# Performance work log

Hardware: AMD Instinct MI355X
Metric: run time of the kernel (lower is better)

The kernel has to match this reference:

```python
import jax, jax.numpy as jnp
import numpy as np

CURV = 1.0          # manifold curvature c
HEADS = 4
HEAD_DIM = 32       # (dim-1) // heads = 128 // 4
SCALE = HEAD_DIM ** -0.5
EPS = 1e-7

N_NODES = 50000
N_EDGES = 800000
D = 128             # tangent feature dim (dim - 1)


def log_origin(x, c):
    """Lorentz log map at the origin o=(1/sqrt(c),0,...); returns spatial (d) part of tangent."""
    sc = jnp.sqrt(c)
    x0 = x[..., 0]
    xs = x[..., 1:]
    norm = jnp.sqrt(jnp.sum(xs * xs, axis=-1) + EPS)         # (N,)
    dist = jnp.arccosh(jnp.maximum(sc * x0, 1.0 + EPS)) / sc  # (N,)
    return (dist / norm)[..., None] * xs                      # (N, d)


def exp_origin(vs, c):
    """Lorentz exp map at origin of tangent vector (0, vs); returns point (N, d+1)."""
    sc = jnp.sqrt(c)
    r = jnp.sqrt(jnp.sum(vs * vs, axis=-1) + EPS)  # (N,)
    arg = sc * r
    x0 = jnp.cosh(arg) / sc
    xs = (jnp.sinh(arg) / arg)[..., None] * vs
    return jnp.concatenate([x0[..., None], xs], axis=-1)


def setup_inputs() -> dict:
    key = jax.random.key(0)
    k1, k2, k3, k4, k5, k6, k7 = jax.random.split(key, 7)
    # valid hyperboloid points: x0 = sqrt(1/c + ||xs||^2)
    xs = 0.5 * jax.random.normal(k1, (N_NODES, D), dtype=jnp.float32)
    x0 = jnp.sqrt(1.0 / CURV + jnp.sum(xs * xs, axis=-1, keepdims=True))
    x = jnp.concatenate([x0, xs], axis=-1)  # (N, d+1)
    edge_index = jax.random.randint(k2, (2, N_EDGES), 0, N_NODES, dtype=jnp.int64)
    s = D ** -0.5
    Wq = s * jax.random.normal(k3, (D, D), dtype=jnp.float32)
    Wk = s * jax.random.normal(k4, (D, D), dtype=jnp.float32)
    Wv = s * jax.random.normal(k5, (D, D), dtype=jnp.float32)
    Wo = s * jax.random.normal(k6, (D, D), dtype=jnp.float32)
    bo = jnp.zeros((D,), dtype=jnp.float32)
    return {"x": x, "edge_index": edge_index, "Wq": Wq, "Wk": Wk, "Wv": Wv, "Wo": Wo, "bo": bo}


def reference(x, edge_index, Wq, Wk, Wv, Wo, bo):
    N = x.shape[0]
    row, col = edge_index[0], edge_index[1]
    # map to tangent space at origin, drop the (zero) time component
    x_tan = log_origin(x, CURV)                       # (N, d)
    Q = (x_tan @ Wq.T).reshape(N, HEADS, HEAD_DIM)
    K = (x_tan @ Wk.T).reshape(N, HEADS, HEAD_DIM)
    V = (x_tan @ Wv.T).reshape(N, HEADS, HEAD_DIM)
    # per-edge attention logits, grouped softmax over incoming edges of each target node (col)
    scores = jnp.einsum('ehd,ehd->eh', Q[col], K[row]) * SCALE   # (E, H)
    m = jax.ops.segment_max(scores, col, num_segments=N)         # (N, H)
    e = jnp.exp(scores - m[col])
    denom = jax.ops.segment_sum(e, col, num_segments=N)          # (N, H)
    att = e / denom[col]                                         # (E, H)
    # weighted scatter-sum of values
    agg = jax.ops.segment_sum(att[..., None] * V[row], col, num_segments=N)  # (N, H, hd)
    agg = agg.reshape(N, HEADS * HEAD_DIM)
    out = agg @ Wo.T + bo                                        # (N, d)
    # lift back: prepend zero time component, exp map at origin
    return exp_origin(out, CURV)                                 # (N, d+1)
```

## Files before the change

kernel.cpp:

```cpp
#include <hip/hip_runtime.h>
#include <hip/hip_fp8.h>
#include <math.h>

#define EPS 1e-7f
#define SCALE 0.17677669529663687f
#define MAXDEG 64
#define BIN_EPT 16
#define BIN_EDGES 4096
#define BUCK_CAP 5120
#define NBUCK_MAX 256

typedef _Float16 half2v __attribute__((ext_vector_type(2)));
typedef _Float16 f16x4 __attribute__((ext_vector_type(4)));
typedef _Float16 f16x8 __attribute__((ext_vector_type(8)));
typedef float f32x4 __attribute__((ext_vector_type(4)));
typedef float f32x2 __attribute__((ext_vector_type(2)));

__device__ __forceinline__ void gload16(const void* g, void* l) {
  __builtin_amdgcn_global_load_lds(
      (const __attribute__((address_space(1))) unsigned int*)g,
      (__attribute__((address_space(3))) unsigned int*)l, 16, 0, 0);
}

__global__ __launch_bounds__(256) void zero_cnt(int* __restrict__ bcnt, int n) {
  int i = blockIdx.x * 256 + threadIdx.x;
  if (i < n) bcnt[i] = 0;
}

__global__ __launch_bounds__(256) void prep_kernel(
    const float* __restrict__ x,
    const float* __restrict__ Wq, const float* __restrict__ Wk,
    const float* __restrict__ Wv, const float* __restrict__ Wo,
    _Float16* __restrict__ Wc, _Float16* __restrict__ Wof,
    _Float16* __restrict__ xt,
    const int* __restrict__ col, const int* __restrict__ row,
    unsigned* __restrict__ staging, int* __restrict__ bcnt,
    int bin_nb, int nbuck, int E, int N) {
  __shared__ int hist[NBUCK_MAX];
  __shared__ int rbase[NBUCK_MAX];
  int b = blockIdx.x;
  int tid = threadIdx.x;
  if (b < bin_nb) {
    int e0 = b * BIN_EDGES;
    if (tid < nbuck) hist[tid] = 0;
    __syncthreads();
    int bkt[BIN_EPT], rk[BIN_EPT];
    unsigned pk[BIN_EPT];
#pragma unroll
    for (int j = 0; j < BIN_EPT; j++) {
      int e = e0 + j * 256 + tid;
      if (e < E) {
        int c = col[e];
        int r = row[e];
        int bb = c >> 8;
        bkt[j] = bb;
        pk[j] = ((unsigned)(c & 255) << 16) | (unsigned)r;
        rk[j] = atomicAdd(&hist[bb], 1);
      } else {
        bkt[j] = -1;
        rk[j] = 0;
        pk[j] = 0;
      }
    }
    __syncthreads();
    if (tid < nbuck) rbase[tid] = atomicAdd(&bcnt[tid], hist[tid]);
    __syncthreads();
#pragma unroll
    for (int j = 0; j < BIN_EPT; j++) {
      if (bkt[j] >= 0) {
        int slot = rbase[bkt[j]] + rk[j];
        if (slot < BUCK_CAP)
          staging[(size_t)bkt[j] * BUCK_CAP + slot] = pk[j];
      }
    }
    return;
  }
  b -= bin_nb;
  if (b < 256) {
    int o = b * 256 + tid;
    int j = o >> 7;
    int i = o & 127;
    if (j < 384) {
      const float* W = (j < 128) ? Wq : (j < 256) ? Wk : Wv;
      Wc[o] = (_Float16)W[(j & 127) * 128 + i];
    } else {
      Wof[(j - 384) * 128 + i] = (_Float16)Wo[(j - 384) * 128 + i];
    }
    return;
  }
  int node = (b - 256) * 4 + (tid >> 6);
  if (node >= N) return;
  int lane = tid & 63;
  float2 xs = *reinterpret_cast<const float2*>(&x[(size_t)node * 129 + 1 + lane * 2]);
  float ss = fmaf(xs.x, xs.x, xs.y * xs.y);
#pragma unroll
  for (int o = 32; o >= 1; o >>= 1) ss += __shfl_xor(ss, o, 64);
  float norm = sqrtf(ss + EPS);
  float x0 = x[(size_t)node * 129];
  float xm = fmaxf(x0, 1.0f + EPS);
  float dist = __logf(xm + sqrtf(fmaxf(fmaf(xm, xm, -1.0f), 0.0f)));
  float sc = dist / norm;
  half2v h;
  h.x = (_Float16)(sc * xs.x);
  h.y = (_Float16)(sc * xs.y);
  *reinterpret_cast<half2v*>(&xt[(size_t)node * 128 + lane * 2]) = h;
}

template <int NCHUNKS, int MODE>
__global__ __launch_bounds__(256, 3) void gemm_mfma(
    const _Float16* __restrict__ A,
    const _Float16* __restrict__ B,
    void* __restrict__ C0, void* __restrict__ C1,
    const float* __restrict__ bias, int M,
    const unsigned* __restrict__ staging, const int* __restrict__ bcnt,
    unsigned short* __restrict__ rml, int* __restrict__ cnt, int Mblocks) {
  __shared__ _Float16 Bs[128 * 128];
  __shared__ __align__(16) unsigned char Cs[16384];
  const int bid = blockIdx.x;
  const int tid = threadIdx.x;

  if (MODE == 0 && bid >= Mblocks) {
    int bk = bid - Mblocks;
    unsigned short* slab = (unsigned short*)Bs;
    int* lc = (int*)Cs;
    lc[tid] = 0;
    __syncthreads();
    int ec = bcnt[bk];
    if (ec > BUCK_CAP) ec = BUCK_CAP;
    const unsigned* sg = staging + (size_t)bk * BUCK_CAP;
    for (int i = tid; i < ec; i += 256) {
      unsigned p = sg[i];
      int nl = p >> 16;
      int pos = atomicAdd(&lc[nl], 1);
      if (pos < MAXDEG) slab[nl * MAXDEG + pos] = (unsigned short)(p & 0xFFFF);
    }
    __syncthreads();
    uint4* gs = (uint4*)(rml + (size_t)bk * 256 * MAXDEG);
    const uint4* ls = (const uint4*)slab;
#pragma unroll
    for (int i = 0; i < 8; i++) gs[i * 256 + tid] = ls[i * 256 + tid];
    int c = lc[tid];
    cnt[bk * 256 + tid] = (c > MAXDEG) ? MAXDEG : c;
    return;
  }

  const int wave = tid >> 6;
  const int lane = tid & 63;
  const int wm = wave >> 1, wn = wave & 1;
  const int lrow = lane & 15, q = lane >> 4;
  const int m0 = bid * 64;

#pragma unroll
  for (int j = 0; j < 4; j++) {
    int slot0 = (j * 4 + wave) * 64;
    int p = slot0 + lane;
    int m = p >> 4;
    int kcl = (p & 15) ^ (m & 15);
    int msrc = m0 + m;
    if (msrc > M - 1) msrc = M - 1;
    gload16(A + (size_t)msrc * 128 + kcl * 8, (char*)Bs + (size_t)slot0 * 16);
  }
  __syncthreads();

  f16x8 afr[2][4];
  {
    const f16x8* Av = (const f16x8*)Bs;
#pragma unroll
    for (int mt = 0; mt < 2; mt++) {
      int m = wm * 32 + mt * 16 + lrow;
#pragma unroll
      for (int s = 0; s < 4; s++) {
        int kc = s * 4 + q;
        afr[mt][s] = Av[m * 16 + (kc ^ (m & 15))];
      }
    }
  }
  __syncthreads();

  auto stageB = [&](int c) {
#pragma unroll
    for (int j = 0; j < 8; j++) {
      int slot0 = (j * 4 + wave) * 64;
      int p = slot0 + lane;
      int n = p >> 4;
      int kcl = (p & 15) ^ (n & 15);
      gload16(B + ((size_t)(c * 128 + n)) * 128 + kcl * 8, (char*)Bs + (size_t)slot0 * 16);
    }
  };
  stageB(0);

  f32x4 acc[2][4];
  for (int c = 0; c < NCHUNKS; c++) {
    __syncthreads();

#pragma unroll
    for (int mt = 0; mt < 2; mt++)
#pragma unroll
      for (int nt = 0; nt < 4; nt++) acc[mt][nt] = (f32x4)0.f;

    const f16x8* Bv = (const f16x8*)Bs;
#pragma unroll
    for (int s = 0; s < 4; s++) {
      int kc = s * 4 + q;
      f16x8 bf[4];
#pragma unroll
      for (int nt = 0; nt < 4; nt++) {
        int n = wn * 64 + nt * 16 + lrow;
        bf[nt] = Bv[n * 16 + (kc ^ (n & 15))];
      }
#pragma unroll
      for (int mt = 0; mt < 2; mt++)
#pragma unroll
        for (int nt = 0; nt < 4; nt++)
          acc[mt][nt] = __builtin_amdgcn_mfma_f32_16x16x32_f16(afr[mt][s], bf[nt], acc[mt][nt], 0, 0, 0);
    }

    if (MODE == 0) {
      if (c == 0) {
#pragma unroll
        for (int mt = 0; mt < 2; mt++)
#pragma unroll
          for (int reg = 0; reg < 4; reg++) {
            int r = wm * 32 + mt * 16 + q * 4 + reg;
            int sw = ((r >> 2) & 3) << 5;
#pragma unroll
            for (int nt = 0; nt < 4; nt++) {
              int cl = wn * 64 + nt * 16 + lrow;
              *(_Float16*)(Cs + r * 256 + ((cl * 2) ^ sw)) = (_Float16)acc[mt][nt][reg];
            }
          }
      } else {
        unsigned char* cb = Cs + ((c == 2) ? 8192 : 0);
#pragma unroll
        for (int mt = 0; mt < 2; mt++) {
          int rb = wm * 32 + mt * 16 + q * 4;
          int sw = ((rb >> 2) & 3) << 5;
#pragma unroll
          for (int nt = 0; nt < 4; nt++) {
            int cl = wn * 64 + nt * 16 + lrow;
            int co = cl ^ sw;
            int p01 = __builtin_amdgcn_cvt_pk_fp8_f32(acc[mt][nt][0], acc[mt][nt][1], 0, false);
            int p23 = __builtin_amdgcn_cvt_pk_fp8_f32(acc[mt][nt][2], acc[mt][nt][3], 0, false);
            cb[(rb + 0) * 128 + co] = (unsigned char)(p01);
            cb[(rb + 1) * 128 + co] = (unsigned char)(p01 >> 8);
            cb[(rb + 2) * 128 + co] = (unsigned char)(p23);
            cb[(rb + 3) * 128 + co] = (unsigned char)(p23 >> 8);
          }
        }
      }
    }
    __syncthreads();
    if (c + 1 < NCHUNKS) stageB(c + 1);
    if (MODE == 0) {
      if (c == 0) {
#pragma unroll
        for (int it = 0; it < 4; it++) {
          int off = it * 4096 + tid * 16;
          int r = off >> 8;
          int bo = off & 255;
          int sw = ((r >> 2) & 3) << 5;
          uint4 v = *(const uint4*)(Cs + r * 256 + (bo ^ sw));
          int rg = m0 + r;
          if (rg < M) *(uint4*)((char*)C0 + (size_t)rg * 256 + bo) = v;
        }
      } else if (c == 2) {
#pragma unroll
        for (int it = 0; it < 8; it++) {
          int off = it * 2048 + tid * 8;
          int r = off >> 8;
          int u4 = (off & 255) >> 1;
          int sw = ((r >> 2) & 3) << 5;
          unsigned kw = *(const unsigned*)(Cs + r * 128 + (u4 ^ sw));
          unsigned vw = *(const unsigned*)(Cs + 8192 + r * 128 + (u4 ^ sw));
          int rg = m0 + r;
          if (rg < M) {
            uint2 o;
            o.x = kw;
            o.y = vw;
            *(uint2*)((char*)C1 + (size_t)rg * 256 + (off & 255)) = o;
          }
        }
      }
    }
  }

  if (MODE == 1) {
    float* out = (float*)C0;
    float* rsum = (float*)Cs;
#pragma unroll
    for (int mt = 0; mt < 2; mt++)
#pragma unroll
      for (int nt = 0; nt < 4; nt++) {
        int cl = wn * 64 + nt * 16 + lrow;
        float b = bias[cl];
#pragma unroll
        for (int reg = 0; reg < 4; reg++) acc[mt][nt][reg] += b;
      }
#pragma unroll
    for (int mt = 0; mt < 2; mt++) {
#pragma unroll
      for (int reg = 0; reg < 4; reg++) {
        float s4 = 0.f;
#pragma unroll
        for (int nt = 0; nt < 4; nt++) s4 = fmaf(acc[mt][nt][reg], acc[mt][nt][reg], s4);
#pragma unroll
        for (int o = 8; o >= 1; o >>= 1) s4 += __shfl_xor(s4, o, 16);
        if (lrow == 0) rsum[(wm * 32 + mt * 16 + q * 4 + reg) * 2 + wn] = s4;
      }
    }
    __syncthreads();
#pragma unroll
    for (int mt = 0; mt < 2; mt++) {
#pragma unroll
      for (int reg = 0; reg < 4; reg++) {
        int rl = wm * 32 + mt * 16 + q * 4 + reg;
        int rg = m0 + rl;
        if (rg < M) {
          float tot = rsum[rl * 2] + rsum[rl * 2 + 1];
          float r = sqrtf(tot + EPS);
          float er = __expf(r);
          float em = __expf(-r);
          float s = (er - em) * 0.5f / r;
#pragma unroll
          for (int nt = 0; nt < 4; nt++) {
            int cl = wn * 64 + nt * 16 + lrow;
            out[(size_t)rg * 129 + 1 + cl] = s * acc[mt][nt][reg];
          }
          if (wn == 0 && lrow == 0) out[(size_t)rg * 129] = (er + em) * 0.5f;
        }
      }
    }
  }
}

__global__ __launch_bounds__(256) void attn_kernel(
    const _Float16* __restrict__ Qb,
    const unsigned char* __restrict__ KVI,
    const unsigned short* __restrict__ rml, const int* __restrict__ cnt,
    _Float16* __restrict__ agg, int N) {
  int node = blockIdx.x * 4 + (threadIdx.x >> 6);
  if (node >= N) return;
  int lane = threadIdx.x & 63;
  int par = lane >> 5;
  int hd = lane & 31;
  int qoff = hd * 4;
  f16x4 qh = *reinterpret_cast<const f16x4*>(Qb + (size_t)node * 128 + qoff);
  float q0 = (float)qh[0], q1 = (float)qh[1], q2 = (float)qh[2], q3 = (float)qh[3];
  int deg = cnt[node];
  if (deg > MAXDEG) deg = MAXDEG;
  const unsigned short* el = rml + (size_t)node * MAXDEG;
  float l = 0.f, av0 = 0.f, av1 = 0.f, av2 = 0.f, av3 = 0.f;

  auto dot = [&](uint2 w, float& p, float& v0, float& v1, float& v2, float& v3) {
    f32x2 k01 = __builtin_amdgcn_cvt_pk_f32_fp8((int)w.x, false);
    f32x2 k23 = __builtin_amdgcn_cvt_pk_f32_fp8((int)w.x, true);
    f32x2 va = __builtin_amdgcn_cvt_pk_f32_fp8((int)w.y, false);
    f32x2 vb = __builtin_amdgcn_cvt_pk_f32_fp8((int)w.y, true);
    v0 = va[0]; v1 = va[1]; v2 = vb[0]; v3 = vb[1];
    p = fmaf(q0, k01[0], fmaf(q1, k01[1], fmaf(q2, k23[0], q3 * k23[1])));
  };

  int i = 0;
  for (; i + 8 <= deg; i += 8) {
    int rA = el[i + par], rB = el[i + 2 + par], rC = el[i + 4 + par], rD = el[i + 6 + par];
    uint2 wA = *reinterpret_cast<const uint2*>(KVI + (size_t)rA * 256 + hd * 8);
    uint2 wB = *reinterpret_cast<const uint2*>(KVI + (size_t)rB * 256 + hd * 8);
    uint2 wC = *reinterpret_cast<const uint2*>(KVI + (size_t)rC * 256 + hd * 8);
    uint2 wD = *reinterpret_cast<const uint2*>(KVI + (size_t)rD * 256 + hd * 8);
    float pA, a4, a5, a6, a7;
    float pB, b4, b5, b6, b7;
    float pC, c4, c5, c6, c7;
    float pD, d4, d5, d6, d7;
    dot(wA, pA, a4, a5, a6, a7);
    dot(wB, pB, b4, b5, b6, b7);
    dot(wC, pC, c4, c5, c6, c7);
    dot(wD, pD, d4, d5, d6, d7);
#pragma unroll
    for (int o = 4; o >= 1; o >>= 1) {
      pA += __shfl_xor(pA, o, 8);
      pB += __shfl_xor(pB, o, 8);
      pC += __shfl_xor(pC, o, 8);
      pD += __shfl_xor(pD, o, 8);
    }
    float eA = __expf(pA * SCALE);
    float eB = __expf(pB * SCALE);
    float eC = __expf(pC * SCALE);
    float eD = __expf(pD * SCALE);
    l += (eA + eB) + (eC + eD);
    av0 = fmaf(eA, a4, av0); av0 = fmaf(eB, b4, av0);
    av1 = fmaf(eA, a5, av1); av1 = fmaf(eB, b5, av1);
    av2 = fmaf(eA, a6, av2); av2 = fmaf(eB, b6, av2);
    av3 = fmaf(eA, a7, av3); av3 = fmaf(eB, b7, av3);
    av0 = fmaf(eC, c4, av0); av0 = fmaf(eD, d4, av0);
    av1 = fmaf(eC, c5, av1); av1 = fmaf(eD, d5, av1);
    av2 = fmaf(eC, c6, av2); av2 = fmaf(eD, d6, av2);
    av3 = fmaf(eC, c7, av3); av3 = fmaf(eD, d7, av3);
  }
  for (; i + 2 <= deg; i += 2) {
    int rA = el[i + par];
    uint2 wA = *reinterpret_cast<const uint2*>(KVI + (size_t)rA * 256 + hd * 8);
    float pA, a4, a5, a6, a7;
    dot(wA, pA, a4, a5, a6, a7);
#pragma unroll
    for (int o = 4; o >= 1; o >>= 1) pA += __shfl_xor(pA, o, 8);
    float eA = __expf(pA * SCALE);
    l += eA;
    av0 = fmaf(eA, a4, av0);
    av1 = fmaf(eA, a5, av1);
    av2 = fmaf(eA, a6, av2);
    av3 = fmaf(eA, a7, av3);
  }
  if (i < deg) {
    int r = el[i];
    uint2 wA = *reinterpret_cast<const uint2*>(KVI + (size_t)r * 256 + hd * 8);
    float pA, a4, a5, a6, a7;
    dot(wA, pA, a4, a5, a6, a7);
#pragma unroll
    for (int o = 4; o >= 1; o >>= 1) pA += __shfl_xor(pA, o, 8);
    float e = __expf(pA * SCALE) * (par ? 0.f : 1.f);
    l += e;
    av0 = fmaf(e, a4, av0);
    av1 = fmaf(e, a5, av1);
    av2 = fmaf(e, a6, av2);
    av3 = fmaf(e, a7, av3);
  }
  l += __shfl_xor(l, 32, 64);
  av0 += __shfl_xor(av0, 32, 64);
  av1 += __shfl_xor(av1, 32, 64);
  av2 += __shfl_xor(av2, 32, 64);
  av3 += __shfl_xor(av3, 32, 64);
  if (par == 0) {
    float inv = (l > 0.f) ? 1.0f / l : 0.f;
    f16x4 o4;
    o4[0] = (_Float16)(av0 * inv);
    o4[1] = (_Float16)(av1 * inv);
    o4[2] = (_Float16)(av2 * inv);
    o4[3] = (_Float16)(av3 * inv);
    *reinterpret_cast<f16x4*>(agg + (size_t)node * 128 + qoff) = o4;
  }
}

extern "C" void kernel_launch(void* const* d_in, const int* in_sizes, int n_in,
                              void* d_out, int out_size, void* d_ws, size_t ws_size,
                              hipStream_t stream) {
  const float* x = (const float*)d_in[0];
  const int* ei = (const int*)d_in[1];
  const float* Wq = (const float*)d_in[2];
  const float* Wk = (const float*)d_in[3];
  const float* Wv = (const float*)d_in[4];
  const float* Wo = (const float*)d_in[5];
  const float* bo = (const float*)d_in[6];
  float* out = (float*)d_out;

  const int N = in_sizes[0] / 129;
  const int E = in_sizes[1] / 2;
  const int* row = ei;
  const int* col = ei + E;

  const int nbuck = (N + 255) >> 8;
  const int bin_nb = (E + BIN_EDGES - 1) / BIN_EDGES;

  char* ws = (char*)d_ws;
  size_t off = 0;
  auto alloc = [&](size_t bytes) -> void* {
    off = (off + 255) & ~(size_t)255;
    void* p = ws + off;
    off += bytes;
    return p;
  };
  _Float16* xtan = (_Float16*)alloc((size_t)N * 128 * 2);
  _Float16* qbuf = (_Float16*)alloc((size_t)N * 128 * 2);
  unsigned char* kvi = (unsigned char*)alloc((size_t)N * 256);
  unsigned short* rml = (unsigned short*)alloc((size_t)nbuck * 256 * MAXDEG * 2);
  int* cnt        = (int*)alloc((size_t)nbuck * 256 * 4);
  unsigned* staging = (unsigned*)alloc((size_t)nbuck * BUCK_CAP * 4);
  int* bcnt       = (int*)alloc((size_t)nbuck * 4);
  _Float16* Wc    = (_Float16*)alloc(384 * 128 * 2);
  _Float16* Wof   = (_Float16*)alloc(128 * 128 * 2);

  const int gemm_nb = (N + 63) / 64;

  zero_cnt<<<(nbuck + 255) / 256, 256, 0, stream>>>(bcnt, nbuck);
  prep_kernel<<<bin_nb + 256 + (N + 3) / 4, 256, 0, stream>>>(
      x, Wq, Wk, Wv, Wo, Wc, Wof, xtan, col, row, staging, bcnt, bin_nb, nbuck,
      E, N);
  gemm_mfma<3, 0><<<gemm_nb + nbuck, 256, 0, stream>>>(
      xtan, Wc, qbuf, kvi, nullptr, N, staging, bcnt, rml, cnt, gemm_nb);
  attn_kernel<<<(N + 3) / 4, 256, 0, stream>>>(qbuf, kvi, rml, cnt, xtan, N);
  gemm_mfma<1, 1><<<gemm_nb, 256, 0, stream>>>(
      xtan, Wof, out, nullptr, bo, N, nullptr, nullptr, nullptr, nullptr, 0);
}
```

Measured before the change: 168.5 us.

## Fuse log map into QKV GEMM and output projection into attention kernel

The Lorentz log map now runs inside the QKV GEMM, written straight into the swizzled LDS A tile, so the separate xtan buffer and its global round trip go away. The attention aggregation is fused with the output projection and exp map: each block handles 64 nodes, stages the aggregated values in LDS, then runs the MFMA against Wo read directly from global memory. This removes one kernel launch and the global write and read of the intermediate agg buffer. In exchange the attention phase now uses 64-node blocks with serial per-wave node loops, so fewer blocks are resident, and the B fragments come from global memory rather than LDS.

```diff
diff --git a/kernel.cpp b/kernel.cpp
--- a/kernel.cpp
+++ b/kernel.cpp
@@ -28,14 +28,12 @@
 }
 
 __global__ __launch_bounds__(256) void prep_kernel(
-    const float* __restrict__ x,
     const float* __restrict__ Wq, const float* __restrict__ Wk,
     const float* __restrict__ Wv, const float* __restrict__ Wo,
     _Float16* __restrict__ Wc, _Float16* __restrict__ Wof,
-    _Float16* __restrict__ xt,
     const int* __restrict__ col, const int* __restrict__ row,
     unsigned* __restrict__ staging, int* __restrict__ bcnt,
-    int bin_nb, int nbuck, int E, int N) {
+    int bin_nb, int nbuck, int E) {
   __shared__ int hist[NBUCK_MAX];
   __shared__ int rbase[NBUCK_MAX];
   int b = blockIdx.x;
@@ -76,42 +74,21 @@
     return;
   }
   b -= bin_nb;
-  if (b < 256) {
-    int o = b * 256 + tid;
-    int j = o >> 7;
-    int i = o & 127;
-    if (j < 384) {
-      const float* W = (j < 128) ? Wq : (j < 256) ? Wk : Wv;
-      Wc[o] = (_Float16)W[(j & 127) * 128 + i];
-    } else {
-      Wof[(j - 384) * 128 + i] = (_Float16)Wo[(j - 384) * 128 + i];
-    }
-    return;
-  }
-  int node = (b - 256) * 4 + (tid >> 6);
-  if (node >= N) return;
-  int lane = tid & 63;
-  float2 xs = *reinterpret_cast<const float2*>(&x[(size_t)node * 129 + 1 + lane * 2]);
-  float ss = fmaf(xs.x, xs.x, xs.y * xs.y);
-#pragma unroll
-  for (int o = 32; o >= 1; o >>= 1) ss += __shfl_xor(ss, o, 64);
-  float norm = sqrtf(ss + EPS);
-  float x0 = x[(size_t)node * 129];
-  float xm = fmaxf(x0, 1.0f + EPS);
-  float dist = __logf(xm + sqrtf(fmaxf(fmaf(xm, xm, -1.0f), 0.0f)));
-  float sc = dist / norm;
-  half2v h;
-  h.x = (_Float16)(sc * xs.x);
-  h.y = (_Float16)(sc * xs.y);
-  *reinterpret_cast<half2v*>(&xt[(size_t)node * 128 + lane * 2]) = h;
+  int o = b * 256 + tid;
+  int j = o >> 7;
+  int i = o & 127;
+  if (j < 384) {
+    const float* W = (j < 128) ? Wq : (j < 256) ? Wk : Wv;
+    Wc[o] = (_Float16)W[(j & 127) * 128 + i];
+  } else {
+    Wof[(j - 384) * 128 + i] = (_Float16)Wo[(j - 384) * 128 + i];
+  }
 }
 
-template <int NCHUNKS, int MODE>
-__global__ __launch_bounds__(256, 3) void gemm_mfma(
-    const _Float16* __restrict__ A,
+__global__ __launch_bounds__(256, 3) void qkv_kernel(
+    const float* __restrict__ x,
     const _Float16* __restrict__ B,
-    void* __restrict__ C0, void* __restrict__ C1,
-    const float* __restrict__ bias, int M,
+    void* __restrict__ C0, void* __restrict__ C1, int M,
     const unsigned* __restrict__ staging, const int* __restrict__ bcnt,
     unsigned short* __restrict__ rml, int* __restrict__ cnt, int Mblocks) {
   __shared__ _Float16 Bs[128 * 128];
@@ -119,7 +96,7 @@
   const int bid = blockIdx.x;
   const int tid = threadIdx.x;
 
-  if (MODE == 0 && bid >= Mblocks) {
+  if (bid >= Mblocks) {
     int bk = bid - Mblocks;
     unsigned short* slab = (unsigned short*)Bs;
     int* lc = (int*)Cs;
@@ -150,15 +127,24 @@
   const int lrow = lane & 15, q = lane >> 4;
   const int m0 = bid * 64;
 
-#pragma unroll
-  for (int j = 0; j < 4; j++) {
-    int slot0 = (j * 4 + wave) * 64;
-    int p = slot0 + lane;
-    int m = p >> 4;
-    int kcl = (p & 15) ^ (m & 15);
+  for (int t = 0; t < 16; t++) {
+    int m = (wave << 4) + t;
     int msrc = m0 + m;
     if (msrc > M - 1) msrc = M - 1;
-    gload16(A + (size_t)msrc * 128 + kcl * 8, (char*)Bs + (size_t)slot0 * 16);
+    const float* xr = x + (size_t)msrc * 129;
+    float2 xs = *reinterpret_cast<const float2*>(xr + 1 + lane * 2);
+    float ss = fmaf(xs.x, xs.x, xs.y * xs.y);
+#pragma unroll
+    for (int o = 32; o >= 1; o >>= 1) ss += __shfl_xor(ss, o, 64);
+    float norm = sqrtf(ss + EPS);
+    float xm = fmaxf(xr[0], 1.0f + EPS);
+    float dist = __logf(xm + sqrtf(fmaxf(fmaf(xm, xm, -1.0f), 0.0f)));
+    float sc = dist / norm;
+    half2v h;
+    h.x = (_Float16)(sc * xs.x);
+    h.y = (_Float16)(sc * xs.y);
+    *reinterpret_cast<half2v*>((char*)Bs + m * 256 +
+                               ((((lane >> 2) ^ (m & 15)) << 4) | ((lane & 3) << 2))) = h;
   }
   __syncthreads();
 
@@ -190,7 +176,7 @@
   stageB(0);
 
   f32x4 acc[2][4];
-  for (int c = 0; c < NCHUNKS; c++) {
+  for (int c = 0; c < 3; c++) {
     __syncthreads();
 
 #pragma unroll
@@ -215,143 +201,91 @@
           acc[mt][nt] = __builtin_amdgcn_mfma_f32_16x16x32_f16(afr[mt][s], bf[nt], acc[mt][nt], 0, 0, 0);
     }
 
-    if (MODE == 0) {
-      if (c == 0) {
-#pragma unroll
-        for (int mt = 0; mt < 2; mt++)
-#pragma unroll
-          for (int reg = 0; reg < 4; reg++) {
-            int r = wm * 32 + mt * 16 + q * 4 + reg;
-            int sw = ((r >> 2) & 3) << 5;
-#pragma unroll
-            for (int nt = 0; nt < 4; nt++) {
-              int cl = wn * 64 + nt * 16 + lrow;
-              *(_Float16*)(Cs + r * 256 + ((cl * 2) ^ sw)) = (_Float16)acc[mt][nt][reg];
-            }
-          }
-      } else {
-        unsigned char* cb = Cs + ((c == 2) ? 8192 : 0);
-#pragma unroll
-        for (int mt = 0; mt < 2; mt++) {
-          int rb = wm * 32 + mt * 16 + q * 4;
-          int sw = ((rb >> 2) & 3) << 5;
+    if (c == 0) {
+#pragma unroll
+      for (int mt = 0; mt < 2; mt++)
+#pragma unroll
+        for (int reg = 0; reg < 4; reg++) {
+          int r = wm * 32 + mt * 16 + q * 4 + reg;
+          int sw = ((r >> 2) & 3) << 5;
 #pragma unroll
           for (int nt = 0; nt < 4; nt++) {
             int cl = wn * 64 + nt * 16 + lrow;
-            int co = cl ^ sw;
-            int p01 = __builtin_amdgcn_cvt_pk_fp8_f32(acc[mt][nt][0], acc[mt][nt][1], 0, false);
-            int p23 = __builtin_amdgcn_cvt_pk_fp8_f32(acc[mt][nt][2], acc[mt][nt][3], 0, false);
-            cb[(rb + 0) * 128 + co] = (unsigned char)(p01);
-            cb[(rb + 1) * 128 + co] = (unsigned char)(p01 >> 8);
-            cb[(rb + 2) * 128 + co] = (unsigned char)(p23);
-            cb[(rb + 3) * 128 + co] = (unsigned char)(p23 >> 8);
+            *(_Float16*)(Cs + r * 256 + ((cl * 2) ^ sw)) = (_Float16)acc[mt][nt][reg];
           }
         }
-      }
-    }
-    __syncthreads();
-    if (c + 1 < NCHUNKS) stageB(c + 1);
-    if (MODE == 0) {
-      if (c == 0) {
-#pragma unroll
-        for (int it = 0; it < 4; it++) {
-          int off = it * 4096 + tid * 16;
-          int r = off >> 8;
-          int bo = off & 255;
-          int sw = ((r >> 2) & 3) << 5;
-          uint4 v = *(const uint4*)(Cs + r * 256 + (bo ^ sw));
-          int rg = m0 + r;
-          if (rg < M) *(uint4*)((char*)C0 + (size_t)rg * 256 + bo) = v;
+    } else {
+      unsigned char* cb = Cs + ((c == 2) ? 8192 : 0);
+#pragma unroll
+      for (int mt = 0; mt < 2; mt++) {
+        int rb = wm * 32 + mt * 16 + q * 4;
+        int sw = ((rb >> 2) & 3) << 5;
+#pragma unroll
+        for (int nt = 0; nt < 4; nt++) {
+          int cl = wn * 64 + nt * 16 + lrow;
+          int co = cl ^ sw;
+          int p01 = __builtin_amdgcn_cvt_pk_fp8_f32(acc[mt][nt][0], acc[mt][nt][1], 0, false);
+          int p23 = __builtin_amdgcn_cvt_pk_fp8_f32(acc[mt][nt][2], acc[mt][nt][3], 0, false);
+          cb[(rb + 0) * 128 + co] = (unsigned char)(p01);
+          cb[(rb + 1) * 128 + co] = (unsigned char)(p01 >> 8);
+          cb[(rb + 2) * 128 + co] = (unsigned char)(p23);
+          cb[(rb + 3) * 128 + co] = (unsigned char)(p23 >> 8);
         }
-      } else if (c == 2) {
-#pragma unroll
-        for (int it = 0; it < 8; it++) {
-          int off = it * 2048 + tid * 8;
-          int r = off >> 8;
-          int u4 = (off & 255) >> 1;
-          int sw = ((r >> 2) & 3) << 5;
-          unsigned kw = *(const unsigned*)(Cs + r * 128 + (u4 ^ sw));
-          unsigned vw = *(const unsigned*)(Cs + 8192 + r * 128 + (u4 ^ sw));
-          int rg = m0 + r;
-          if (rg < M) {
-            uint2 o;
-            o.x = kw;
-            o.y = vw;
-            *(uint2*)((char*)C1 + (size_t)rg * 256 + (off & 255)) = o;
-          }
+      }
+    }
+    __syncthreads();
+    if (c + 1 < 3) stageB(c + 1);
+    if (c == 0) {
+#pragma unroll
+      for (int it = 0; it < 4; it++) {
+        int off = it * 4096 + tid * 16;
+        int r = off >> 8;
+        int bo = off & 255;
+        int sw = ((r >> 2) & 3) << 5;
+        uint4 v = *(const uint4*)(Cs + r * 256 + (bo ^ sw));
+        int rg = m0 + r;
+        if (rg < M) *(uint4*)((char*)C0 + (size_t)rg * 256 + bo) = v;
+      }
+    } else if (c == 2) {
+#pragma unroll
+      for (int it = 0; it < 8; it++) {
+        int off = it * 2048 + tid * 8;
+        int r = off >> 8;
+        int u4 = (off & 255) >> 1;
+        int sw = ((r >> 2) & 3) << 5;
+        unsigned kw = *(const unsigned*)(Cs + r * 128 + (u4 ^ sw));
+        unsigned vw = *(const unsigned*)(Cs + 8192 + r * 128 + (u4 ^ sw));
+        int rg = m0 + r;
+        if (rg < M) {
+          uint2 o;
+          o.x = kw;
+          o.y = vw;
+          *(uint2*)((char*)C1 + (size_t)rg * 256 + (off & 255)) = o;
         }
       }
     }
   }
-
-  if (MODE == 1) {
-    float* out = (float*)C0;
-    float* rsum = (float*)Cs;
-#pragma unroll
-    for (int mt = 0; mt < 2; mt++)
-#pragma unroll
-      for (int nt = 0; nt < 4; nt++) {
-        int cl = wn * 64 + nt * 16 + lrow;
-        float b = bias[cl];
-#pragma unroll
-        for (int reg = 0; reg < 4; reg++) acc[mt][nt][reg] += b;
-      }
-#pragma unroll
-    for (int mt = 0; mt < 2; mt++) {
-#pragma unroll
-      for (int reg = 0; reg < 4; reg++) {
-        float s4 = 0.f;
-#pragma unroll
-        for (int nt = 0; nt < 4; nt++) s4 = fmaf(acc[mt][nt][reg], acc[mt][nt][reg], s4);
-#pragma unroll
-        for (int o = 8; o >= 1; o >>= 1) s4 += __shfl_xor(s4, o, 16);
-        if (lrow == 0) rsum[(wm * 32 + mt * 16 + q * 4 + reg) * 2 + wn] = s4;
-      }
-    }
-    __syncthreads();
-#pragma unroll
-    for (int mt = 0; mt < 2; mt++) {
-#pragma unroll
-      for (int reg = 0; reg < 4; reg++) {
-        int rl = wm * 32 + mt * 16 + q * 4 + reg;
-        int rg = m0 + rl;
-        if (rg < M) {
-          float tot = rsum[rl * 2] + rsum[rl * 2 + 1];
-          float r = sqrtf(tot + EPS);
-          float er = __expf(r);
-          float em = __expf(-r);
-          float s = (er - em) * 0.5f / r;
-#pragma unroll
-          for (int nt = 0; nt < 4; nt++) {
-            int cl = wn * 64 + nt * 16 + lrow;
-            out[(size_t)rg * 129 + 1 + cl] = s * acc[mt][nt][reg];
-          }
-          if (wn == 0 && lrow == 0) out[(size_t)rg * 129] = (er + em) * 0.5f;
-        }
-      }
-    }
-  }
 }
 
-__global__ __launch_bounds__(256) void attn_kernel(
+__global__ __launch_bounds__(256) void attn_out_kernel(
     const _Float16* __restrict__ Qb,
     const unsigned char* __restrict__ KVI,
     const unsigned short* __restrict__ rml, const int* __restrict__ cnt,
-    _Float16* __restrict__ agg, int N) {
-  int node = blockIdx.x * 4 + (threadIdx.x >> 6);
-  if (node >= N) return;
-  int lane = threadIdx.x & 63;
-  int par = lane >> 5;
-  int hd = lane & 31;
-  int qoff = hd * 4;
-  f16x4 qh = *reinterpret_cast<const f16x4*>(Qb + (size_t)node * 128 + qoff);
-  float q0 = (float)qh[0], q1 = (float)qh[1], q2 = (float)qh[2], q3 = (float)qh[3];
-  int deg = cnt[node];
-  if (deg > MAXDEG) deg = MAXDEG;
-  const unsigned short* el = rml + (size_t)node * MAXDEG;
-  float l = 0.f, av0 = 0.f, av1 = 0.f, av2 = 0.f, av3 = 0.f;
-
-  auto dot = [&](uint2 w, float& p, float& v0, float& v1, float& v2, float& v3) {
+    const _Float16* __restrict__ Wof,
+    const float* __restrict__ bias,
+    float* __restrict__ out, int N) {
+  __shared__ __align__(16) _Float16 Ags[64 * 128];
+  __shared__ float rsum[64 * 2];
+  const int tid = threadIdx.x;
+  const int wave = tid >> 6;
+  const int lane = tid & 63;
+  const int blk = blockIdx.x;
+  const int par = lane >> 5;
+  const int hd = lane & 31;
+  const int qoff = hd * 4;
+
+  auto dot = [&](uint2 w, float q0, float q1, float q2, float q3, float& p,
+                 float& v0, float& v1, float& v2, float& v3) {
     f32x2 k01 = __builtin_amdgcn_cvt_pk_f32_fp8((int)w.x, false);
     f32x2 k23 = __builtin_amdgcn_cvt_pk_f32_fp8((int)w.x, true);
     f32x2 va = __builtin_amdgcn_cvt_pk_f32_fp8((int)w.y, false);
@@ -360,83 +294,171 @@
     p = fmaf(q0, k01[0], fmaf(q1, k01[1], fmaf(q2, k23[0], q3 * k23[1])));
   };
 
-  int i = 0;
-  for (; i + 8 <= deg; i += 8) {
-    int rA = el[i + par], rB = el[i + 2 + par], rC = el[i + 4 + par], rD = el[i + 6 + par];
-    uint2 wA = *reinterpret_cast<const uint2*>(KVI + (size_t)rA * 256 + hd * 8);
-    uint2 wB = *reinterpret_cast<const uint2*>(KVI + (size_t)rB * 256 + hd * 8);
-    uint2 wC = *reinterpret_cast<const uint2*>(KVI + (size_t)rC * 256 + hd * 8);
-    uint2 wD = *reinterpret_cast<const uint2*>(KVI + (size_t)rD * 256 + hd * 8);
-    float pA, a4, a5, a6, a7;
-    float pB, b4, b5, b6, b7;
-    float pC, c4, c5, c6, c7;
-    float pD, d4, d5, d6, d7;
-    dot(wA, pA, a4, a5, a6, a7);
-    dot(wB, pB, b4, b5, b6, b7);
-    dot(wC, pC, c4, c5, c6, c7);
-    dot(wD, pD, d4, d5, d6, d7);
-#pragma unroll
-    for (int o = 4; o >= 1; o >>= 1) {
-      pA += __shfl_xor(pA, o, 8);
-      pB += __shfl_xor(pB, o, 8);
-      pC += __shfl_xor(pC, o, 8);
-      pD += __shfl_xor(pD, o, 8);
-    }
-    float eA = __expf(pA * SCALE);
-    float eB = __expf(pB * SCALE);
-    float eC = __expf(pC * SCALE);
-    float eD = __expf(pD * SCALE);
-    l += (eA + eB) + (eC + eD);
-    av0 = fmaf(eA, a4, av0); av0 = fmaf(eB, b4, av0);
-    av1 = fmaf(eA, a5, av1); av1 = fmaf(eB, b5, av1);
-    av2 = fmaf(eA, a6, av2); av2 = fmaf(eB, b6, av2);
-    av3 = fmaf(eA, a7, av3); av3 = fmaf(eB, b7, av3);
-    av0 = fmaf(eC, c4, av0); av0 = fmaf(eD, d4, av0);
-    av1 = fmaf(eC, c5, av1); av1 = fmaf(eD, d5, av1);
-    av2 = fmaf(eC, c6, av2); av2 = fmaf(eD, d6, av2);
-    av3 = fmaf(eC, c7, av3); av3 = fmaf(eD, d7, av3);
-  }
-  for (; i + 2 <= deg; i += 2) {
-    int rA = el[i + par];
-    uint2 wA = *reinterpret_cast<const uint2*>(KVI + (size_t)rA * 256 + hd * 8);
-    float pA, a4, a5, a6, a7;
-    dot(wA, pA, a4, a5, a6, a7);
-#pragma unroll
-    for (int o = 4; o >= 1; o >>= 1) pA += __shfl_xor(pA, o, 8);
-    float eA = __expf(pA * SCALE);
-    l += eA;
-    av0 = fmaf(eA, a4, av0);
-    av1 = fmaf(eA, a5, av1);
-    av2 = fmaf(eA, a6, av2);
-    av3 = fmaf(eA, a7, av3);
-  }
-  if (i < deg) {
-    int r = el[i];
-    uint2 wA = *reinterpret_cast<const uint2*>(KVI + (size_t)r * 256 + hd * 8);
-    float pA, a4, a5, a6, a7;
-    dot(wA, pA, a4, a5, a6, a7);
-#pragma unroll
-    for (int o = 4; o >= 1; o >>= 1) pA += __shfl_xor(pA, o, 8);
-    float e = __expf(pA * SCALE) * (par ? 0.f : 1.f);
-    l += e;
-    av0 = fmaf(e, a4, av0);
-    av1 = fmaf(e, a5, av1);
-    av2 = fmaf(e, a6, av2);
-    av3 = fmaf(e, a7, av3);
-  }
-  l += __shfl_xor(l, 32, 64);
-  av0 += __shfl_xor(av0, 32, 64);
-  av1 += __shfl_xor(av1, 32, 64);
-  av2 += __shfl_xor(av2, 32, 64);
-  av3 += __shfl_xor(av3, 32, 64);
-  if (par == 0) {
-    float inv = (l > 0.f) ? 1.0f / l : 0.f;
-    f16x4 o4;
-    o4[0] = (_Float16)(av0 * inv);
-    o4[1] = (_Float16)(av1 * inv);
-    o4[2] = (_Float16)(av2 * inv);
-    o4[3] = (_Float16)(av3 * inv);
-    *reinterpret_cast<f16x4*>(agg + (size_t)node * 128 + qoff) = o4;
+  for (int t = 0; t < 16; t++) {
+    int nl = (wave << 4) + t;
+    int node = blk * 64 + nl;
+    float l = 0.f, av0 = 0.f, av1 = 0.f, av2 = 0.f, av3 = 0.f;
+    if (node < N) {
+      f16x4 qh = *reinterpret_cast<const f16x4*>(Qb + (size_t)node * 128 + qoff);
+      float q0 = (float)qh[0], q1 = (float)qh[1], q2 = (float)qh[2], q3 = (float)qh[3];
+      int deg = cnt[node];
+      if (deg > MAXDEG) deg = MAXDEG;
+      const unsigned short* el = rml + (size_t)node * MAXDEG;
+      int i = 0;
+      for (; i + 8 <= deg; i += 8) {
+        int rA = el[i + par], rB = el[i + 2 + par], rC = el[i + 4 + par], rD = el[i + 6 + par];
+        uint2 wA = *reinterpret_cast<const uint2*>(KVI + (size_t)rA * 256 + hd * 8);
+        uint2 wB = *reinterpret_cast<const uint2*>(KVI + (size_t)rB * 256 + hd * 8);
+        uint2 wC = *reinterpret_cast<const uint2*>(KVI + (size_t)rC * 256 + hd * 8);
+        uint2 wD = *reinterpret_cast<const uint2*>(KVI + (size_t)rD * 256 + hd * 8);
+        float pA, a4, a5, a6, a7;
+        float pB, b4, b5, b6, b7;
+        float pC, c4, c5, c6, c7;
+        float pD, d4, d5, d6, d7;
+        dot(wA, q0, q1, q2, q3, pA, a4, a5, a6, a7);
+        dot(wB, q0, q1, q2, q3, pB, b4, b5, b6, b7);
+        dot(wC, q0, q1, q2, q3, pC, c4, c5, c6, c7);
+        dot(wD, q0, q1, q2, q3, pD, d4, d5, d6, d7);
+#pragma unroll
+        for (int o = 4; o >= 1; o >>= 1) {
+          pA += __shfl_xor(pA, o, 8);
+          pB += __shfl_xor(pB, o, 8);
+          pC += __shfl_xor(pC, o, 8);
+          pD += __shfl_xor(pD, o, 8);
+        }
+        float eA = __expf(pA * SCALE);
+        float eB = __expf(pB * SCALE);
+        float eC = __expf(pC * SCALE);
+        float eD = __expf(pD * SCALE);
+        l += (eA + eB) + (eC + eD);
+        av0 = fmaf(eA, a4, av0); av0 = fmaf(eB, b4, av0);
+        av1 = fmaf(eA, a5, av1); av1 = fmaf(eB, b5, av1);
+        av2 = fmaf(eA, a6, av2); av2 = fmaf(eB, b6, av2);
+        av3 = fmaf(eA, a7, av3); av3 = fmaf(eB, b7, av3);
+        av0 = fmaf(eC, c4, av0); av0 = fmaf(eD, d4, av0);
+        av1 = fmaf(eC, c5, av1); av1 = fmaf(eD, d5, av1);
+        av2 = fmaf(eC, c6, av2); av2 = fmaf(eD, d6, av2);
+        av3 = fmaf(eC, c7, av3); av3 = fmaf(eD, d7, av3);
+      }
+      for (; i + 2 <= deg; i += 2) {
+        int rA = el[i + par];
+        uint2 wA = *reinterpret_cast<const uint2*>(KVI + (size_t)rA * 256 + hd * 8);
+        float pA, a4, a5, a6, a7;
+        dot(wA, q0, q1, q2, q3, pA, a4, a5, a6, a7);
+#pragma unroll
+        for (int o = 4; o >= 1; o >>= 1) pA += __shfl_xor(pA, o, 8);
+        float eA = __expf(pA * SCALE);
+        l += eA;
+        av0 = fmaf(eA, a4, av0);
+        av1 = fmaf(eA, a5, av1);
+        av2 = fmaf(eA, a6, av2);
+        av3 = fmaf(eA, a7, av3);
+      }
+      if (i < deg) {
+        int r = el[i];
+        uint2 wA = *reinterpret_cast<const uint2*>(KVI + (size_t)r * 256 + hd * 8);
+        float pA, a4, a5, a6, a7;
+        dot(wA, q0, q1, q2, q3, pA, a4, a5, a6, a7);
+#pragma unroll
+        for (int o = 4; o >= 1; o >>= 1) pA += __shfl_xor(pA, o, 8);
+        float e = __expf(pA * SCALE) * (par ? 0.f : 1.f);
+        l += e;
+        av0 = fmaf(e, a4, av0);
+        av1 = fmaf(e, a5, av1);
+        av2 = fmaf(e, a6, av2);
+        av3 = fmaf(e, a7, av3);
+      }
+      l += __shfl_xor(l, 32, 64);
+      av0 += __shfl_xor(av0, 32, 64);
+      av1 += __shfl_xor(av1, 32, 64);
+      av2 += __shfl_xor(av2, 32, 64);
+      av3 += __shfl_xor(av3, 32, 64);
+    }
+    if (par == 0) {
+      float inv = (l > 0.f) ? 1.0f / l : 0.f;
+      f16x4 o4;
+      o4[0] = (_Float16)(av0 * inv);
+      o4[1] = (_Float16)(av1 * inv);
+      o4[2] = (_Float16)(av2 * inv);
+      o4[3] = (_Float16)(av3 * inv);
+      *reinterpret_cast<f16x4*>((char*)Ags + nl * 256 +
+                                ((((hd >> 1) ^ (nl & 15)) << 4) | ((hd & 1) << 3))) = o4;
+    }
+  }
+  __syncthreads();
+
+  const int wm = wave >> 1, wn = wave & 1;
+  const int lrow = lane & 15, q = lane >> 4;
+  f32x4 acc[2][4];
+#pragma unroll
+  for (int mt = 0; mt < 2; mt++)
+#pragma unroll
+    for (int nt = 0; nt < 4; nt++) acc[mt][nt] = (f32x4)0.f;
+
+  const f16x8* Av = (const f16x8*)Ags;
+#pragma unroll
+  for (int s = 0; s < 4; s++) {
+    int kc = s * 4 + q;
+    f16x8 af[2], bf[4];
+#pragma unroll
+    for (int mt = 0; mt < 2; mt++) {
+      int m = wm * 32 + mt * 16 + lrow;
+      af[mt] = Av[m * 16 + (kc ^ (m & 15))];
+    }
+#pragma unroll
+    for (int nt = 0; nt < 4; nt++) {
+      int n = wn * 64 + nt * 16 + lrow;
+      bf[nt] = *reinterpret_cast<const f16x8*>(Wof + (size_t)n * 128 + kc * 8);
+    }
+#pragma unroll
+    for (int mt = 0; mt < 2; mt++)
+#pragma unroll
+      for (int nt = 0; nt < 4; nt++)
+        acc[mt][nt] = __builtin_amdgcn_mfma_f32_16x16x32_f16(af[mt], bf[nt], acc[mt][nt], 0, 0, 0);
+  }
+
+#pragma unroll
+  for (int mt = 0; mt < 2; mt++)
+#pragma unroll
+    for (int nt = 0; nt < 4; nt++) {
+      int cl = wn * 64 + nt * 16 + lrow;
+      float b = bias[cl];
+#pragma unroll
+      for (int reg = 0; reg < 4; reg++) acc[mt][nt][reg] += b;
+    }
+#pragma unroll
+  for (int mt = 0; mt < 2; mt++) {
+#pragma unroll
+    for (int reg = 0; reg < 4; reg++) {
+      float s4 = 0.f;
+#pragma unroll
+      for (int nt = 0; nt < 4; nt++) s4 = fmaf(acc[mt][nt][reg], acc[mt][nt][reg], s4);
+#pragma unroll
+      for (int o = 8; o >= 1; o >>= 1) s4 += __shfl_xor(s4, o, 16);
+      if (lrow == 0) rsum[(wm * 32 + mt * 16 + q * 4 + reg) * 2 + wn] = s4;
+    }
+  }
+  __syncthreads();
+#pragma unroll
+  for (int mt = 0; mt < 2; mt++) {
+#pragma unroll
+    for (int reg = 0; reg < 4; reg++) {
+      int rl = wm * 32 + mt * 16 + q * 4 + reg;
+      int rg = blk * 64 + rl;
+      if (rg < N) {
+        float tot = rsum[rl * 2] + rsum[rl * 2 + 1];
+        float r = sqrtf(tot + EPS);
+        float er = __expf(r);
+        float em = __expf(-r);
+        float s = (er - em) * 0.5f / r;
+#pragma unroll
+        for (int nt = 0; nt < 4; nt++) {
+          int cl = wn * 64 + nt * 16 + lrow;
+          out[(size_t)rg * 129 + 1 + cl] = s * acc[mt][nt][reg];
+        }
+        if (wn == 0 && lrow == 0) out[(size_t)rg * 129] = (er + em) * 0.5f;
+      }
+    }
   }
 }
 
@@ -468,7 +490,6 @@
     off += bytes;
     return p;
   };
-  _Float16* xtan = (_Float16*)alloc((size_t)N * 128 * 2);
   _Float16* qbuf = (_Float16*)alloc((size_t)N * 128 * 2);
   unsigned char* kvi = (unsigned char*)alloc((size_t)N * 256);
   unsigned short* rml = (unsigned short*)alloc((size_t)nbuck * 256 * MAXDEG * 2);
@@ -481,12 +502,9 @@
   const int gemm_nb = (N + 63) / 64;
 
   zero_cnt<<<(nbuck + 255) / 256, 256, 0, stream>>>(bcnt, nbuck);
-  prep_kernel<<<bin_nb + 256 + (N + 3) / 4, 256, 0, stream>>>(
-      x, Wq, Wk, Wv, Wo, Wc, Wof, xtan, col, row, staging, bcnt, bin_nb, nbuck,
-      E, N);
-  gemm_mfma<3, 0><<<gemm_nb + nbuck, 256, 0, stream>>>(
-      xtan, Wc, qbuf, kvi, nullptr, N, staging, bcnt, rml, cnt, gemm_nb);
-  attn_kernel<<<(N + 3) / 4, 256, 0, stream>>>(qbuf, kvi, rml, cnt, xtan, N);
-  gemm_mfma<1, 1><<<gemm_nb, 256, 0, stream>>>(
-      xtan, Wof, out, nullptr, bo, N, nullptr, nullptr, nullptr, nullptr, 0);
+  prep_kernel<<<bin_nb + 256, 256, 0, stream>>>(
+      Wq, Wk, Wv, Wo, Wc, Wof, col, row, staging, bcnt, bin_nb, nbuck, E);
+  qkv_kernel<<<gemm_nb + nbuck, 256, 0, stream>>>(
+      x, Wc, qbuf, kvi, N, staging, bcnt, rml, cnt, gemm_nb);
+  attn_out_kernel<<<gemm_nb, 256, 0, stream>>>(qbuf, kvi, rml, cnt, Wof, bo, out, N);
 }
```

After: 201.4 us. +19.5%, slower.
